# Kernel optimization log

Hardware: AMD Instinct MI355X
Metric: run time of the kernel (lower is better)

The kernel has to match this reference:

```python
import jax, jax.numpy as jnp
import numpy as np

N, IPI, OPI, OPO = 20000, 128, 64, 16

def setup_inputs() -> dict:
    key = jax.random.key(0)
    k1, k2, k3, k4 = jax.random.split(key, 4)
    admat = jax.random.uniform(k1, (N, N), dtype=jnp.float32)
    features = jax.random.normal(k2, (N, IPI), dtype=jnp.float32)
    W1 = jax.random.normal(k3, (IPI, OPI), dtype=jnp.float32) * (1.0 / np.sqrt(IPI))
    W2 = jax.random.normal(k4, (OPI, OPO), dtype=jnp.float32) * (1.0 / np.sqrt(OPI))
    return {"admat": admat, "features": features, "W1": W1, "W2": W2}

def reference(admat, features, W1, W2):
    # layer1: A @ (X @ W1), thin-first ordering to minimize FLOPs/traffic
    h = jax.nn.relu(admat @ (features @ W1))          # [N, OPI]
    logits = admat @ (h @ W2)                          # [N, OPO]
    return jax.nn.softmax(logits, axis=1)
```

## Files before the change

kernel.cpp:

```cpp
#include <hip/hip_runtime.h>
#include <hip/hip_bf16.h>

#define NROWS 20000
#define IPI 128
#define OPI 64
#define OPO 16
#define BK 256
#define BK2 1024
#define A8S 20480

typedef __attribute__((ext_vector_type(8))) short bf16x8;
typedef __attribute__((ext_vector_type(4))) float f32x4;
typedef __attribute__((ext_vector_type(2))) unsigned int u32x2;
typedef __attribute__((ext_vector_type(4))) unsigned int u32x4;

static __device__ __forceinline__ unsigned short f2bf(float f) {
    __hip_bfloat16 h = __float2bfloat16(f);
    return *reinterpret_cast<unsigned short*>(&h);
}
static __device__ __forceinline__ unsigned pk2(float a, float b) {
    return (unsigned)f2bf(a) | ((unsigned)f2bf(b) << 16);
}
static __device__ __forceinline__ unsigned pk4_fp8(float a, float b, float c, float d) {
    int v = __builtin_amdgcn_cvt_pk_fp8_f32(a, b, 0, false);
    v = __builtin_amdgcn_cvt_pk_fp8_f32(c, d, v, true);
    return (unsigned)v;
}
static __device__ __forceinline__ unsigned char f2fp8(float a) {
    return (unsigned char)(pk4_fp8(a, 0.f, 0.f, 0.f) & 0xff);
}

__global__ __launch_bounds__(256)
void k_xw1(const float* __restrict__ X, const float* __restrict__ W1,
           unsigned short* __restrict__ Bt) {
    __shared__ float w1[IPI * OPI];
    const int t = threadIdx.x;
    for (int i = t * 4; i < IPI * OPI; i += 1024)
        *(float4*)&w1[i] = *(const float4*)&W1[i];
    __syncthreads();

    const int r  = blockIdx.x * 16 + (t >> 4);
    const int c4 = (t & 15) * 4;
    const float* xr = X + (size_t)r * IPI;
    float4 acc = make_float4(0.f, 0.f, 0.f, 0.f);
    #pragma unroll 8
    for (int k = 0; k < IPI; ++k) {
        const float x = xr[k];
        const float4 w = *(const float4*)&w1[k * OPI + c4];
        acc.x = fmaf(x, w.x, acc.x);
        acc.y = fmaf(x, w.y, acc.y);
        acc.z = fmaf(x, w.z, acc.z);
        acc.w = fmaf(x, w.w, acc.w);
    }
    Bt[(size_t)(c4 + 0) * NROWS + r] = f2bf(acc.x);
    Bt[(size_t)(c4 + 1) * NROWS + r] = f2bf(acc.y);
    Bt[(size_t)(c4 + 2) * NROWS + r] = f2bf(acc.z);
    Bt[(size_t)(c4 + 3) * NROWS + r] = f2bf(acc.w);
}

__global__ __launch_bounds__(256)
void k_gemm1(const float* __restrict__ A, const unsigned short* __restrict__ Bt,
             float* __restrict__ Out, unsigned char* __restrict__ A8, int KC) {
    __shared__ unsigned short As[64 * BK];
    __shared__ unsigned short Bs[64 * BK];
    const int t    = threadIdx.x;
    const int lane = t & 63;
    const int wid  = t >> 6;
    const int lrow = lane & 15;
    const int lk   = lane >> 4;
    const int brow    = blockIdx.x * 64;
    const int k_begin = blockIdx.y * KC;
    const int k_end   = min(NROWS, k_begin + KC);

    const int sc_c = lane >> 1;
    const int sc_h = (lane & 1) * 4;

    f32x4 acc[4];
    #pragma unroll
    for (int n = 0; n < 4; ++n) acc[n] = (f32x4){0.f, 0.f, 0.f, 0.f};

    for (int kt = k_begin; kt < k_end; kt += BK) {
        const int  kg  = kt + lane * 4;
        const bool kok = kg < k_end;

        f32x4 va[16];
        u32x2 vb[16];
        #pragma unroll
        for (int i = 0; i < 16; ++i) {
            const int grow = brow + wid * 16 + i;
            va[i] = (f32x4){0.f, 0.f, 0.f, 0.f};
            if (kok && grow < NROWS)
                va[i] = __builtin_nontemporal_load(
                    (const f32x4*)(A + (size_t)grow * NROWS + kg));
            vb[i] = (u32x2){0u, 0u};
            if (kok)
                vb[i] = *(const u32x2*)(Bt + (size_t)(wid * 16 + i) * NROWS + kg);
        }
        #pragma unroll
        for (int i = 0; i < 16; ++i) {
            const int r = wid * 16 + i;
            const int grow = brow + r;
            u32x2 u;
            u[0] = pk2(va[i][0], va[i][1]);
            u[1] = pk2(va[i][2], va[i][3]);
            const int slot = (sc_c ^ (r & 7)) * 8 + sc_h;
            *(u32x2*)&As[r * BK + slot] = u;
            *(u32x2*)&Bs[r * BK + slot] = vb[i];
            if (kok && grow < NROWS)
                __builtin_nontemporal_store(
                    pk4_fp8(va[i][0], va[i][1], va[i][2], va[i][3]),
                    (unsigned*)(A8 + (size_t)grow * A8S + kg));
        }
        __syncthreads();

        #pragma unroll
        for (int h = 0; h < 8; ++h) {
            const int c  = h * 4 + lk;
            const int sc = (c & ~7) | ((c & 7) ^ (lrow & 7));
            const bf16x8 a = *(const bf16x8*)&As[(wid * 16 + lrow) * BK + sc * 8];
            #pragma unroll
            for (int n = 0; n < 4; ++n) {
                const bf16x8 b = *(const bf16x8*)&Bs[(n * 16 + lrow) * BK + sc * 8];
                acc[n] = __builtin_amdgcn_mfma_f32_16x16x32_bf16(a, b, acc[n], 0, 0, 0);
            }
        }
        __syncthreads();
    }

    float* outp = Out + (size_t)blockIdx.y * NROWS * OPI;
    const int r0 = (lane >> 4) * 4;
    #pragma unroll
    for (int n = 0; n < 4; ++n)
        #pragma unroll
        for (int r = 0; r < 4; ++r) {
            const int grow = brow + wid * 16 + r0 + r;
            if (grow < NROWS)
                outp[(size_t)grow * OPI + n * 16 + lrow] = acc[n][r];
        }
}

__global__ __launch_bounds__(256)
void k_hw2(const float* __restrict__ Hpart, const float* __restrict__ W2,
           unsigned char* __restrict__ Zt8, int S1) {
    __shared__ float w2[OPI * OPO];
    __shared__ float hs[16 * 68];
    const int t = threadIdx.x;
    if (t * 4 < OPI * OPO)
        *(float4*)&w2[t * 4] = *(const float4*)&W2[t * 4];

    const int r  = t >> 4;
    const int c4 = (t & 15) * 4;
    const size_t rowg = (size_t)blockIdx.x * 16 + r;

    float4 h = make_float4(0.f, 0.f, 0.f, 0.f);
    for (int s = 0; s < S1; ++s) {
        const float4 v = *(const float4*)&Hpart[((size_t)s * NROWS + rowg) * OPI + c4];
        h.x += v.x; h.y += v.y; h.z += v.z; h.w += v.w;
    }
    hs[r * 68 + c4 + 0] = fmaxf(h.x, 0.f);
    hs[r * 68 + c4 + 1] = fmaxf(h.y, 0.f);
    hs[r * 68 + c4 + 2] = fmaxf(h.z, 0.f);
    hs[r * 68 + c4 + 3] = fmaxf(h.w, 0.f);
    __syncthreads();

    const int c = t & 15;
    float z = 0.f;
    #pragma unroll 8
    for (int k = 0; k < OPI; ++k)
        z = fmaf(hs[r * 68 + k], w2[k * OPO + c], z);
    Zt8[(size_t)c * NROWS + rowg] = f2fp8(z * 0.25f);
}

__global__ __launch_bounds__(256)
void k_gemm2(const unsigned char* __restrict__ A8,
             const unsigned char* __restrict__ Zt8,
             float* __restrict__ Out, int KC) {
    __shared__ unsigned char As[64 * BK2];
    __shared__ unsigned char Bs[16 * BK2];
    const int t    = threadIdx.x;
    const int lane = t & 63;
    const int wid  = t >> 6;
    const int lrow = lane & 15;
    const int lk   = lane >> 4;
    const int brow    = blockIdx.x * 64;
    const int k_begin = blockIdx.y * KC;
    const int k_end   = min(NROWS, k_begin + KC);

    f32x4 acc = (f32x4){0.f, 0.f, 0.f, 0.f};

    for (int kt = k_begin; kt < k_end; kt += BK2) {
        const int  kgA = kt + lane * 16;
        const bool okA = kgA < k_end;
        u32x4 va[16];
        #pragma unroll
        for (int i = 0; i < 16; ++i) {
            const int grow = brow + wid * 16 + i;
            va[i] = (u32x4){0u, 0u, 0u, 0u};
            if (okA && grow < NROWS)
                va[i] = __builtin_nontemporal_load(
                    (const u32x4*)(A8 + (size_t)grow * A8S + kgA));
        }
        #pragma unroll
        for (int i = 0; i < 16; ++i) {
            const int r  = wid * 16 + i;
            const int c  = lane;
            const int sc = (c & ~7) | ((c & 7) ^ (r & 7));
            *(u32x4*)&As[r * BK2 + sc * 16] = va[i];
        }
        {
            const int col = t >> 4;
            const int off = (t & 15) * 64;
            const unsigned char* zp = Zt8 + (size_t)col * NROWS + kt + off;
            #pragma unroll
            for (int j = 0; j < 4; ++j) {
                const int kg = kt + off + j * 16;
                u32x4 v = (u32x4){0u, 0u, 0u, 0u};
                if (kg < k_end) v = *(const u32x4*)(zp + j * 16);
                const int c  = (off >> 4) + j;
                const int sc = (c & ~7) | ((c & 7) ^ (col & 7));
                *(u32x4*)&Bs[col * BK2 + sc * 16] = v;
            }
        }
        __syncthreads();

        #pragma unroll
        for (int h = 0; h < 32; ++h) {
            const int k0   = h * 32 + lk * 8;
            const int c    = k0 >> 4;
            const int hb   = k0 & 15;
            const int sc   = (c & ~7) | ((c & 7) ^ (lrow & 7));
            const long long a = *(const long long*)&As[(wid * 16 + lrow) * BK2 + sc * 16 + hb];
            const long long b = *(const long long*)&Bs[lrow * BK2 + sc * 16 + hb];
            acc = __builtin_amdgcn_mfma_f32_16x16x32_fp8_fp8(a, b, acc, 0, 0, 0);
        }
        __syncthreads();
    }

    float* outp = Out + (size_t)blockIdx.y * NROWS * OPO;
    const int r0 = (lane >> 4) * 4;
    #pragma unroll
    for (int r = 0; r < 4; ++r) {
        const int grow = brow + wid * 16 + r0 + r;
        if (grow < NROWS) outp[(size_t)grow * OPO + lrow] = acc[r];
    }
}

__global__ __launch_bounds__(256)
void k_softmax(const float* __restrict__ Lpart, float* __restrict__ out, int S2) {
    const int t = threadIdx.x;
    const size_t base = (size_t)blockIdx.x * 256;
    float v = 0.f;
    for (int s = 0; s < S2; ++s)
        v += Lpart[(size_t)s * NROWS * OPO + base + t];
    v *= 4.f;
    float m = v;
    #pragma unroll
    for (int d = 8; d >= 1; d >>= 1) m = fmaxf(m, __shfl_xor(m, d, 16));
    const float e = expf(v - m);
    float sum = e;
    #pragma unroll
    for (int d = 8; d >= 1; d >>= 1) sum += __shfl_xor(sum, d, 16);
    out[base + t] = e / sum;
}

extern "C" void kernel_launch(void* const* d_in, const int* in_sizes, int n_in,
                              void* d_out, int out_size, void* d_ws, size_t ws_size,
                              hipStream_t stream) {
    const float* A  = (const float*)d_in[0];
    const float* X  = (const float*)d_in[1];
    const float* W1 = (const float*)d_in[2];
    const float* W2 = (const float*)d_in[3];
    float* out = (float*)d_out;

    auto al = [](size_t x) { return (x + 1023) & ~(size_t)1023; };
    const size_t a8_b = al((size_t)NROWS * A8S);
    const size_t bt_b = al((size_t)OPI * NROWS * 2);
    const size_t z8_b = al((size_t)OPO * NROWS);

    int S1 = 8, S2 = 8;
    auto need = [&](int s1, int s2) {
        return a8_b + bt_b + z8_b +
               ((size_t)s1 * NROWS * OPI + (size_t)s2 * NROWS * OPO) * sizeof(float);
    };
    while ((S1 > 1 || S2 > 1) && need(S1, S2) > ws_size) {
        if (S1 > 1) S1 >>= 1;
        if (S2 > 1) S2 >>= 1;
    }

    char* p = (char*)d_ws;
    unsigned char*  A8  = (unsigned char*)p;
    unsigned short* Bt  = (unsigned short*)(p + a8_b);
    unsigned char*  Zt8 = (unsigned char*)(p + a8_b + bt_b);
    float* H = (float*)(p + a8_b + bt_b + z8_b);
    float* L = H + (size_t)S1 * NROWS * OPI;

    const int MT  = (NROWS + 63) / 64;
    const int KC1 = ((((NROWS + S1 - 1) / S1) + BK - 1) / BK) * BK;
    const int KC2 = ((((NROWS + S2 - 1) / S2) + 511) & ~511);

    k_xw1<<<dim3(NROWS / 16), 256, 0, stream>>>(X, W1, Bt);
    k_gemm1<<<dim3(MT, S1), 256, 0, stream>>>(A, Bt, H, A8, KC1);
    k_hw2<<<dim3(NROWS / 16), 256, 0, stream>>>(H, W2, Zt8, S1);
    k_gemm2<<<dim3(MT, S2), 256, 0, stream>>>(A8, Zt8, L, KC2);
    k_softmax<<<dim3(NROWS * OPO / 256), 256, 0, stream>>>(L, out, S2);
}
```

Before: 559.0 us.

## Software-pipeline global loads in both GEMM kernels via register prefetch

Both the bf16 GEMM1 and fp8 GEMM2 main loops now prefetch the next K tile's global data into a second register set while the current tile's MFMAs run from shared memory. In GEMM1 the fp8 write-back of A is also moved after the barrier so it overlaps with compute. The goal is to hide global memory latency behind the matrix work in this memory-bound kernel. The cost is doubled register usage for the staging arrays, which may lower occupancy or cause spills.

New measurement: 551.3 us. No clear change (-1.4%).

```diff
diff --git a/kernel.cpp b/kernel.cpp
--- a/kernel.cpp
+++ b/kernel.cpp
@@ -79,12 +79,12 @@
     #pragma unroll
     for (int n = 0; n < 4; ++n) acc[n] = (f32x4){0.f, 0.f, 0.f, 0.f};
 
-    for (int kt = k_begin; kt < k_end; kt += BK) {
-        const int  kg  = kt + lane * 4;
+    f32x4 va[16], vna[16];
+    u32x2 vb[16], vnb[16];
+
+    {
+        const int  kg  = k_begin + lane * 4;
         const bool kok = kg < k_end;
-
-        f32x4 va[16];
-        u32x2 vb[16];
         #pragma unroll
         for (int i = 0; i < 16; ++i) {
             const int grow = brow + wid * 16 + i;
@@ -96,22 +96,46 @@
             if (kok)
                 vb[i] = *(const u32x2*)(Bt + (size_t)(wid * 16 + i) * NROWS + kg);
         }
+    }
+
+    for (int kt = k_begin; kt < k_end; kt += BK) {
         #pragma unroll
         for (int i = 0; i < 16; ++i) {
             const int r = wid * 16 + i;
-            const int grow = brow + r;
             u32x2 u;
             u[0] = pk2(va[i][0], va[i][1]);
             u[1] = pk2(va[i][2], va[i][3]);
             const int slot = (sc_c ^ (r & 7)) * 8 + sc_h;
             *(u32x2*)&As[r * BK + slot] = u;
             *(u32x2*)&Bs[r * BK + slot] = vb[i];
-            if (kok && grow < NROWS)
-                __builtin_nontemporal_store(
-                    pk4_fp8(va[i][0], va[i][1], va[i][2], va[i][3]),
-                    (unsigned*)(A8 + (size_t)grow * A8S + kg));
         }
         __syncthreads();
+
+        {
+            const int  kgn  = kt + BK + lane * 4;
+            const bool nok  = kgn < k_end;
+            #pragma unroll
+            for (int i = 0; i < 16; ++i) {
+                const int grow = brow + wid * 16 + i;
+                vna[i] = (f32x4){0.f, 0.f, 0.f, 0.f};
+                if (nok && grow < NROWS)
+                    vna[i] = __builtin_nontemporal_load(
+                        (const f32x4*)(A + (size_t)grow * NROWS + kgn));
+                vnb[i] = (u32x2){0u, 0u};
+                if (nok)
+                    vnb[i] = *(const u32x2*)(Bt + (size_t)(wid * 16 + i) * NROWS + kgn);
+            }
+            const int  kg  = kt + lane * 4;
+            const bool kok = kg < k_end;
+            #pragma unroll
+            for (int i = 0; i < 16; ++i) {
+                const int grow = brow + wid * 16 + i;
+                if (kok && grow < NROWS)
+                    __builtin_nontemporal_store(
+                        pk4_fp8(va[i][0], va[i][1], va[i][2], va[i][3]),
+                        (unsigned*)(A8 + (size_t)grow * A8S + kg));
+            }
+        }
 
         #pragma unroll
         for (int h = 0; h < 8; ++h) {
@@ -125,6 +149,9 @@
             }
         }
         __syncthreads();
+
+        #pragma unroll
+        for (int i = 0; i < 16; ++i) { va[i] = vna[i]; vb[i] = vnb[i]; }
     }
 
     float* outp = Out + (size_t)blockIdx.y * NROWS * OPI;
@@ -188,10 +215,15 @@
 
     f32x4 acc = (f32x4){0.f, 0.f, 0.f, 0.f};
 
-    for (int kt = k_begin; kt < k_end; kt += BK2) {
-        const int  kgA = kt + lane * 16;
+    const int zcol = t >> 4;
+    const int zoff = (t & 15) * 64;
+
+    u32x4 va[16], vna[16];
+    u32x4 vz[4],  vnz[4];
+
+    {
+        const int  kgA = k_begin + lane * 16;
         const bool okA = kgA < k_end;
-        u32x4 va[16];
         #pragma unroll
         for (int i = 0; i < 16; ++i) {
             const int grow = brow + wid * 16 + i;
@@ -201,27 +233,49 @@
                     (const u32x4*)(A8 + (size_t)grow * A8S + kgA));
         }
         #pragma unroll
+        for (int j = 0; j < 4; ++j) {
+            const int kg = k_begin + zoff + j * 16;
+            vz[j] = (u32x4){0u, 0u, 0u, 0u};
+            if (kg < k_end)
+                vz[j] = *(const u32x4*)(Zt8 + (size_t)zcol * NROWS + kg);
+        }
+    }
+
+    for (int kt = k_begin; kt < k_end; kt += BK2) {
+        #pragma unroll
         for (int i = 0; i < 16; ++i) {
             const int r  = wid * 16 + i;
             const int c  = lane;
             const int sc = (c & ~7) | ((c & 7) ^ (r & 7));
             *(u32x4*)&As[r * BK2 + sc * 16] = va[i];
         }
+        #pragma unroll
+        for (int j = 0; j < 4; ++j) {
+            const int c  = (zoff >> 4) + j;
+            const int sc = (c & ~7) | ((c & 7) ^ (zcol & 7));
+            *(u32x4*)&Bs[zcol * BK2 + sc * 16] = vz[j];
+        }
+        __syncthreads();
+
         {
-            const int col = t >> 4;
-            const int off = (t & 15) * 64;
-            const unsigned char* zp = Zt8 + (size_t)col * NROWS + kt + off;
+            const int  kgn = kt + BK2 + lane * 16;
+            const bool nok = kgn < k_end;
+            #pragma unroll
+            for (int i = 0; i < 16; ++i) {
+                const int grow = brow + wid * 16 + i;
+                vna[i] = (u32x4){0u, 0u, 0u, 0u};
+                if (nok && grow < NROWS)
+                    vna[i] = __builtin_nontemporal_load(
+                        (const u32x4*)(A8 + (size_t)grow * A8S + kgn));
+            }
             #pragma unroll
             for (int j = 0; j < 4; ++j) {
-                const int kg = kt + off + j * 16;
-                u32x4 v = (u32x4){0u, 0u, 0u, 0u};
-                if (kg < k_end) v = *(const u32x4*)(zp + j * 16);
-                const int c  = (off >> 4) + j;
-                const int sc = (c & ~7) | ((c & 7) ^ (col & 7));
-                *(u32x4*)&Bs[col * BK2 + sc * 16] = v;
-            }
-        }
-        __syncthreads();
+                const int kg = kt + BK2 + zoff + j * 16;
+                vnz[j] = (u32x4){0u, 0u, 0u, 0u};
+                if (kg < k_end)
+                    vnz[j] = *(const u32x4*)(Zt8 + (size_t)zcol * NROWS + kg);
+            }
+        }
 
         #pragma unroll
         for (int h = 0; h < 32; ++h) {
@@ -234,6 +288,11 @@
             acc = __builtin_amdgcn_mfma_f32_16x16x32_fp8_fp8(a, b, acc, 0, 0, 0);
         }
         __syncthreads();
+
+        #pragma unroll
+        for (int i = 0; i < 16; ++i) va[i] = vna[i];
+        #pragma unroll
+        for (int j = 0; j < 4; ++j)  vz[j] = vnz[j];
     }
 
     float* outp = Out + (size_t)blockIdx.y * NROWS * OPO;
```
